# Performance work log

Measured on AMD Instinct MI355X. Metric: run time of the kernel, lower is better.

Reference implementation:

```python
import jax, jax.numpy as jnp
import numpy as np

N = 100000   # nodes (in_ch)
D = 128      # emb_ch
E = 1600000  # nonzeros in A_hat
RATE = 0.1   # dropout rate


def setup_inputs() -> dict:
    key = jax.random.key(0)
    k1, k2, k3, k4, k5, k6 = jax.random.split(key, 6)
    x = jnp.arange(N, dtype=jnp.int64) if jax.config.jax_enable_x64 else jnp.arange(N, dtype=jnp.int32)
    rows = jax.random.randint(k1, (E,), 0, N)
    cols = jax.random.randint(k2, (E,), 0, N)
    A_vals = jax.random.uniform(k3, (E,), dtype=jnp.float32)
    # xavier_uniform for [N, D]: bound = sqrt(6/(N+D))
    bound = float(np.sqrt(6.0 / (N + D)))
    emb_weight = jax.random.uniform(k4, (N, D), jnp.float32, -bound, bound)
    u1 = jax.random.uniform(k5, (N, D), dtype=jnp.float32)
    u2 = jax.random.uniform(k6, (N, D), dtype=jnp.float32)
    return {"x": x, "rows": rows, "cols": cols, "A_vals": A_vals,
            "emb_weight": emb_weight, "u1": u1, "u2": u2}


def _dropout(h, u):
    keep = (u >= RATE).astype(h.dtype)
    return h * keep / (1.0 - RATE)


def _spmm(rows, cols, vals, h):
    # out[i] = sum_{e: rows[e]==i} vals[e] * h[cols[e]]  -- COO SpMM
    msgs = vals[:, None] * h[cols]  # [E, D]
    return jax.ops.segment_sum(msgs, rows, num_segments=N)


def reference(x, rows, cols, A_vals, emb_weight, u1, u2):
    h0 = emb_weight[x]                       # embedding lookup [N, D]
    h1 = _spmm(rows, cols, A_vals, _dropout(h0, u1))
    h2 = _spmm(rows, cols, A_vals, _dropout(h1, u2))
    return (h0 + h1 + h2) / 3.0
```

## Files before the change

### kernel.cpp

```cpp
#include <hip/hip_runtime.h>

#define DD 128
#define SCAN_CHUNK 1024

struct __align__(8) Edge { int c; float v; };

__device__ __forceinline__ unsigned short f2bf(float f) {
    unsigned int u = __float_as_uint(f);
    u = u + 0x7fffu + ((u >> 16) & 1u);
    return (unsigned short)(u >> 16);
}
__device__ __forceinline__ float bf_lo(unsigned int p) { return __uint_as_float(p << 16); }
__device__ __forceinline__ float bf_hi(unsigned int p) { return __uint_as_float(p & 0xffff0000u); }


__global__ __launch_bounds__(256) void k_zero(int* __restrict__ p, int n) {
    int i = blockIdx.x * 256 + threadIdx.x;
    if (i < n) p[i] = 0;
}

__global__ __launch_bounds__(256) void k_hist(const int* __restrict__ rows,
                                              int* __restrict__ cnt,
                                              int* __restrict__ rank, int E) {
    int e = blockIdx.x * 256 + threadIdx.x;
    if (e < E) rank[e] = atomicAdd(&cnt[rows[e]], 1);
}

__global__ __launch_bounds__(256) void k_scan1(int* __restrict__ data,
                                               int* __restrict__ bsum, int n) {
    __shared__ int s[256];
    int tid = threadIdx.x;
    int base = blockIdx.x * SCAN_CHUNK + tid * 4;
    int v0 = 0, v1 = 0, v2 = 0, v3 = 0;
    if (base + 0 < n) v0 = data[base + 0];
    if (base + 1 < n) v1 = data[base + 1];
    if (base + 2 < n) v2 = data[base + 2];
    if (base + 3 < n) v3 = data[base + 3];
    int tsum = v0 + v1 + v2 + v3;
    s[tid] = tsum;
    __syncthreads();
    for (int off = 1; off < 256; off <<= 1) {
        int t = (tid >= off) ? s[tid - off] : 0;
        __syncthreads();
        s[tid] += t;
        __syncthreads();
    }
    int excl = s[tid] - tsum;
    if (tid == 255) bsum[blockIdx.x] = s[255];
    if (base + 0 < n) data[base + 0] = excl;
    if (base + 1 < n) data[base + 1] = excl + v0;
    if (base + 2 < n) data[base + 2] = excl + v0 + v1;
    if (base + 3 < n) data[base + 3] = excl + v0 + v1 + v2;
}

__global__ __launch_bounds__(256) void k_scan23(int* __restrict__ data,
                                                const int* __restrict__ bsum,
                                                int nb, int n) {
    __shared__ int s[1024];
    int tid = threadIdx.x;
    for (int i = tid; i < nb; i += 256) s[i] = bsum[i];
    __syncthreads();
    if (tid == 0) {
        int run = 0;
        for (int i = 0; i < nb; ++i) { int t = s[i]; s[i] = run; run += t; }
    }
    __syncthreads();
    int i = blockIdx.x * 256 + tid;
    if (i < n) data[i] += s[i >> 10];
}

__global__ __launch_bounds__(256) void k_scatter(const int* __restrict__ rows,
                                                 const int* __restrict__ cols,
                                                 const float* __restrict__ vals,
                                                 const int* __restrict__ rowstart,
                                                 const int* __restrict__ rank,
                                                 Edge* __restrict__ ev, int E) {
    int e = blockIdx.x * 256 + threadIdx.x;
    if (e >= E) return;
    int r = rows[e];
    Edge ed;
    ed.c = cols[e];
    ed.v = vals[e];
    ev[rowstart[r] + rank[e]] = ed;
}


__global__ __launch_bounds__(256) void k_drop_bf(const float* __restrict__ src,
                                                 const float* __restrict__ u,
                                                 ushort* __restrict__ g, int total4) {
    int i = blockIdx.x * 256 + threadIdx.x;
    if (i >= total4) return;
    float4 h = ((const float4*)src)[i];
    float4 uu = ((const float4*)u)[i];
    const float s = 1.0f / 0.9f;
    ushort4 o;
    o.x = f2bf((uu.x >= 0.1f) ? h.x * s : 0.0f);
    o.y = f2bf((uu.y >= 0.1f) ? h.y * s : 0.0f);
    o.z = f2bf((uu.z >= 0.1f) ? h.z * s : 0.0f);
    o.w = f2bf((uu.w >= 0.1f) ? h.w * s : 0.0f);
    ((ushort4*)g)[i] = o;
}

template <int MODE>
__global__ __launch_bounds__(256) void k_gather(const int* __restrict__ rowstart,
                                                const Edge* __restrict__ ev,
                                                const ushort* __restrict__ srcb,
                                                const float* __restrict__ u2,
                                                const float* __restrict__ emb,
                                                const float* __restrict__ h1in,
                                                float* __restrict__ dst,
                                                ushort* __restrict__ g2,
                                                int N, int E) {
    int t = blockIdx.x * 256 + threadIdx.x;
    int row = t >> 5;
    int lane = t & 31;
    if (row >= N) return;
    int start = rowstart[row];
    int end = (row == N - 1) ? E : rowstart[row + 1];
    const uint2* s2 = (const uint2*)srcb;
    float ax = 0.f, ay = 0.f, az = 0.f, aw = 0.f;
    int e = start;
    for (; e + 4 <= end; e += 4) {
        Edge e0 = ev[e + 0];
        Edge e1 = ev[e + 1];
        Edge e2 = ev[e + 2];
        Edge e3 = ev[e + 3];
        uint2 p0 = s2[((size_t)e0.c << 5) + lane];
        uint2 p1 = s2[((size_t)e1.c << 5) + lane];
        uint2 p2 = s2[((size_t)e2.c << 5) + lane];
        uint2 p3 = s2[((size_t)e3.c << 5) + lane];
        ax = fmaf(e0.v, bf_lo(p0.x), ax); ay = fmaf(e0.v, bf_hi(p0.x), ay);
        az = fmaf(e0.v, bf_lo(p0.y), az); aw = fmaf(e0.v, bf_hi(p0.y), aw);
        ax = fmaf(e1.v, bf_lo(p1.x), ax); ay = fmaf(e1.v, bf_hi(p1.x), ay);
        az = fmaf(e1.v, bf_lo(p1.y), az); aw = fmaf(e1.v, bf_hi(p1.y), aw);
        ax = fmaf(e2.v, bf_lo(p2.x), ax); ay = fmaf(e2.v, bf_hi(p2.x), ay);
        az = fmaf(e2.v, bf_lo(p2.y), az); aw = fmaf(e2.v, bf_hi(p2.y), aw);
        ax = fmaf(e3.v, bf_lo(p3.x), ax); ay = fmaf(e3.v, bf_hi(p3.x), ay);
        az = fmaf(e3.v, bf_lo(p3.y), az); aw = fmaf(e3.v, bf_hi(p3.y), aw);
    }
    for (; e < end; ++e) {
        Edge ed = ev[e];
        uint2 p = s2[((size_t)ed.c << 5) + lane];
        ax = fmaf(ed.v, bf_lo(p.x), ax); ay = fmaf(ed.v, bf_hi(p.x), ay);
        az = fmaf(ed.v, bf_lo(p.y), az); aw = fmaf(ed.v, bf_hi(p.y), aw);
    }
    size_t o = ((size_t)row << 7) + (size_t)lane * 4;
    if (MODE == 1) {
        *(float4*)(dst + o) = make_float4(ax, ay, az, aw);
        float4 uu = *(const float4*)(u2 + o);
        const float s = 1.0f / 0.9f;
        ushort4 gg;
        gg.x = f2bf((uu.x >= 0.1f) ? ax * s : 0.0f);
        gg.y = f2bf((uu.y >= 0.1f) ? ay * s : 0.0f);
        gg.z = f2bf((uu.z >= 0.1f) ? az * s : 0.0f);
        gg.w = f2bf((uu.w >= 0.1f) ? aw * s : 0.0f);
        *(ushort4*)(g2 + o) = gg;
    } else {
        float4 e4 = *(const float4*)(emb + o);
        float4 h4 = *(const float4*)(h1in + o);
        const float t3 = 1.0f / 3.0f;
        float4 r;
        r.x = (e4.x + h4.x + ax) * t3;
        r.y = (e4.y + h4.y + ay) * t3;
        r.z = (e4.z + h4.z + az) * t3;
        r.w = (e4.w + h4.w + aw) * t3;
        *(float4*)(dst + o) = r;
    }
}


extern "C" void kernel_launch(void* const* d_in, const int* in_sizes, int n_in,
                              void* d_out, int out_size, void* d_ws, size_t ws_size,
                              hipStream_t stream) {
    const int* rows = (const int*)d_in[1];
    const int* cols = (const int*)d_in[2];
    const float* vals = (const float*)d_in[3];
    const float* emb = (const float*)d_in[4];
    const float* u1 = (const float*)d_in[5];
    const float* u2 = (const float*)d_in[6];
    float* out = (float*)d_out;

    const int N = in_sizes[0];
    const int E = in_sizes[1];
    const size_t ND = (size_t)N * DD;

    char* ws = (char*)d_ws;
    ushort* g1 = (ushort*)ws;  ws += ND * sizeof(ushort);
    ushort* g2 = (ushort*)ws;  ws += ND * sizeof(ushort);
    float* h1  = (float*)ws;   ws += ND * sizeof(float);
    int* cnt   = (int*)ws;     ws += (size_t)N * sizeof(int);
    int* rank  = (int*)ws;     ws += (size_t)E * sizeof(int);
    Edge* ev   = (Edge*)ws;    ws += (size_t)E * sizeof(Edge);
    int* bsum  = (int*)ws;

    const int total4 = (int)(ND / 4);
    const int gridElem = (total4 + 255) / 256;
    const int gridE = (E + 255) / 256;
    const int gridN = (N + 255) / 256;
    const int nScanBlocks = (N + SCAN_CHUNK - 1) / SCAN_CHUNK;
    const int gridRow = (int)(((size_t)N * 32 + 255) / 256);

    k_zero<<<gridN, 256, 0, stream>>>(cnt, N);
    k_hist<<<gridE, 256, 0, stream>>>(rows, cnt, rank, E);
    k_scan1<<<nScanBlocks, 256, 0, stream>>>(cnt, bsum, N);
    k_scan23<<<gridN, 256, 0, stream>>>(cnt, bsum, nScanBlocks, N);
    k_scatter<<<gridE, 256, 0, stream>>>(rows, cols, vals, cnt, rank, ev, E);

    k_drop_bf<<<gridElem, 256, 0, stream>>>(emb, u1, g1, total4);
    k_gather<1><<<gridRow, 256, 0, stream>>>(cnt, ev, g1, u2, nullptr, nullptr, h1, g2, N, E);
    k_gather<2><<<gridRow, 256, 0, stream>>>(cnt, ev, g2, nullptr, emb, h1, out, nullptr, N, E);
}
```

Measured before the change: 452.7 us.

## Switch gathered features to fp16, widen gather lanes, add nontemporal loads/stores

Stores the dropout-applied features and the intermediate h1 as fp16 instead of bf16/fp32, which halves the h1 round trip. The gather kernel now uses 16 lanes per row, each loading 16 bytes (8 halves), and unrolls by 8 edges to put more loads in flight. Nontemporal load/store hints are added across the preprocessing, dropout and epilogue streams. Storing h1 in fp16 adds rounding error to the final output, and fp16 has a narrower exponent range than bf16.

```diff
diff --git a/kernel.cpp b/kernel.cpp
--- a/kernel.cpp
+++ b/kernel.cpp
@@ -1,17 +1,28 @@
 #include <hip/hip_runtime.h>
+#include <hip/hip_fp16.h>
 
 #define DD 128
 #define SCAN_CHUNK 1024
 
+typedef float          f32x4 __attribute__((ext_vector_type(4)));
+typedef unsigned int   u32x4 __attribute__((ext_vector_type(4)));
+typedef unsigned int   u32x2 __attribute__((ext_vector_type(2)));
+typedef unsigned short u16x8 __attribute__((ext_vector_type(8)));
+
 struct __align__(8) Edge { int c; float v; };
 
-__device__ __forceinline__ unsigned short f2bf(float f) {
-    unsigned int u = __float_as_uint(f);
-    u = u + 0x7fffu + ((u >> 16) & 1u);
-    return (unsigned short)(u >> 16);
-}
-__device__ __forceinline__ float bf_lo(unsigned int p) { return __uint_as_float(p << 16); }
-__device__ __forceinline__ float bf_hi(unsigned int p) { return __uint_as_float(p & 0xffff0000u); }
+__device__ __forceinline__ unsigned short f2h(float f) {
+    return __half_as_ushort(__float2half(f));
+}
+__device__ __forceinline__ float2 up2(unsigned int u) {
+    __half2 h = *reinterpret_cast<const __half2*>(&u);
+    return __half22float2(h);
+}
+
+template <typename T>
+__device__ __forceinline__ T ldnt(const T* p) { return __builtin_nontemporal_load(p); }
+template <typename T>
+__device__ __forceinline__ void stnt(T* p, T v) { __builtin_nontemporal_store(v, p); }
 
 
 __global__ __launch_bounds__(256) void k_zero(int* __restrict__ p, int n) {
@@ -23,7 +34,11 @@
                                               int* __restrict__ cnt,
                                               int* __restrict__ rank, int E) {
     int e = blockIdx.x * 256 + threadIdx.x;
-    if (e < E) rank[e] = atomicAdd(&cnt[rows[e]], 1);
+    if (e < E) {
+        int r = ldnt(rows + e);
+        int old = atomicAdd(&cnt[r], 1);
+        stnt(rank + e, old);
+    }
 }
 
 __global__ __launch_bounds__(256) void k_scan1(int* __restrict__ data,
@@ -77,94 +92,125 @@
                                                  Edge* __restrict__ ev, int E) {
     int e = blockIdx.x * 256 + threadIdx.x;
     if (e >= E) return;
-    int r = rows[e];
+    int r = ldnt(rows + e);
     Edge ed;
-    ed.c = cols[e];
-    ed.v = vals[e];
+    ed.c = ldnt(cols + e);
+    ed.v = ldnt(vals + e);
     ev[rowstart[r] + rank[e]] = ed;
 }
 
 
-__global__ __launch_bounds__(256) void k_drop_bf(const float* __restrict__ src,
-                                                 const float* __restrict__ u,
-                                                 ushort* __restrict__ g, int total4) {
+__global__ __launch_bounds__(256) void k_drop_h(const float* __restrict__ src,
+                                                const float* __restrict__ u,
+                                                ushort* __restrict__ g, int total8) {
     int i = blockIdx.x * 256 + threadIdx.x;
-    if (i >= total4) return;
-    float4 h = ((const float4*)src)[i];
-    float4 uu = ((const float4*)u)[i];
+    if (i >= total8) return;
+    const f32x4* s4 = (const f32x4*)src;
+    const f32x4* u4 = (const f32x4*)u;
+    f32x4 hA = ldnt(s4 + 2 * (size_t)i);
+    f32x4 hB = ldnt(s4 + 2 * (size_t)i + 1);
+    f32x4 uA = ldnt(u4 + 2 * (size_t)i);
+    f32x4 uB = ldnt(u4 + 2 * (size_t)i + 1);
     const float s = 1.0f / 0.9f;
-    ushort4 o;
-    o.x = f2bf((uu.x >= 0.1f) ? h.x * s : 0.0f);
-    o.y = f2bf((uu.y >= 0.1f) ? h.y * s : 0.0f);
-    o.z = f2bf((uu.z >= 0.1f) ? h.z * s : 0.0f);
-    o.w = f2bf((uu.w >= 0.1f) ? h.w * s : 0.0f);
-    ((ushort4*)g)[i] = o;
+    u16x8 o;
+    o[0] = f2h((uA.x >= 0.1f) ? hA.x * s : 0.0f);
+    o[1] = f2h((uA.y >= 0.1f) ? hA.y * s : 0.0f);
+    o[2] = f2h((uA.z >= 0.1f) ? hA.z * s : 0.0f);
+    o[3] = f2h((uA.w >= 0.1f) ? hA.w * s : 0.0f);
+    o[4] = f2h((uB.x >= 0.1f) ? hB.x * s : 0.0f);
+    o[5] = f2h((uB.y >= 0.1f) ? hB.y * s : 0.0f);
+    o[6] = f2h((uB.z >= 0.1f) ? hB.z * s : 0.0f);
+    o[7] = f2h((uB.w >= 0.1f) ? hB.w * s : 0.0f);
+    ((u16x8*)g)[i] = o;
 }
 
 template <int MODE>
 __global__ __launch_bounds__(256) void k_gather(const int* __restrict__ rowstart,
                                                 const Edge* __restrict__ ev,
-                                                const ushort* __restrict__ srcb,
+                                                const ushort* __restrict__ srch,
                                                 const float* __restrict__ u2,
                                                 const float* __restrict__ emb,
-                                                const float* __restrict__ h1in,
-                                                float* __restrict__ dst,
+                                                const ushort* __restrict__ p16in,
+                                                ushort* __restrict__ p16out,
                                                 ushort* __restrict__ g2,
+                                                float* __restrict__ out,
                                                 int N, int E) {
     int t = blockIdx.x * 256 + threadIdx.x;
-    int row = t >> 5;
-    int lane = t & 31;
+    int row = t >> 4;
+    int lane = t & 15;
     if (row >= N) return;
     int start = rowstart[row];
     int end = (row == N - 1) ? E : rowstart[row + 1];
-    const uint2* s2 = (const uint2*)srcb;
-    float ax = 0.f, ay = 0.f, az = 0.f, aw = 0.f;
+    const u32x4* __restrict__ s4 = (const u32x4*)srch;
+    float a0 = 0.f, a1 = 0.f, a2 = 0.f, a3 = 0.f;
+    float a4 = 0.f, a5 = 0.f, a6 = 0.f, a7 = 0.f;
+
+#define LDE(i) Edge E##i; { u32x2 q_ = ldnt((const u32x2*)(ev + e + i)); \
+                            E##i.c = (int)q_.x; E##i.v = __uint_as_float(q_.y); }
+#define GQ(i)  u32x4 q##i = s4[((size_t)E##i.c << 4) + lane];
+#define ACC(i) { float vv = E##i.v; \
+        float2 w0 = up2(q##i.x), w1 = up2(q##i.y), w2 = up2(q##i.z), w3 = up2(q##i.w); \
+        a0 = fmaf(vv, w0.x, a0); a1 = fmaf(vv, w0.y, a1); \
+        a2 = fmaf(vv, w1.x, a2); a3 = fmaf(vv, w1.y, a3); \
+        a4 = fmaf(vv, w2.x, a4); a5 = fmaf(vv, w2.y, a5); \
+        a6 = fmaf(vv, w3.x, a6); a7 = fmaf(vv, w3.y, a7); }
+
     int e = start;
-    for (; e + 4 <= end; e += 4) {
-        Edge e0 = ev[e + 0];
-        Edge e1 = ev[e + 1];
-        Edge e2 = ev[e + 2];
-        Edge e3 = ev[e + 3];
-        uint2 p0 = s2[((size_t)e0.c << 5) + lane];
-        uint2 p1 = s2[((size_t)e1.c << 5) + lane];
-        uint2 p2 = s2[((size_t)e2.c << 5) + lane];
-        uint2 p3 = s2[((size_t)e3.c << 5) + lane];
-        ax = fmaf(e0.v, bf_lo(p0.x), ax); ay = fmaf(e0.v, bf_hi(p0.x), ay);
-        az = fmaf(e0.v, bf_lo(p0.y), az); aw = fmaf(e0.v, bf_hi(p0.y), aw);
-        ax = fmaf(e1.v, bf_lo(p1.x), ax); ay = fmaf(e1.v, bf_hi(p1.x), ay);
-        az = fmaf(e1.v, bf_lo(p1.y), az); aw = fmaf(e1.v, bf_hi(p1.y), aw);
-        ax = fmaf(e2.v, bf_lo(p2.x), ax); ay = fmaf(e2.v, bf_hi(p2.x), ay);
-        az = fmaf(e2.v, bf_lo(p2.y), az); aw = fmaf(e2.v, bf_hi(p2.y), aw);
-        ax = fmaf(e3.v, bf_lo(p3.x), ax); ay = fmaf(e3.v, bf_hi(p3.x), ay);
-        az = fmaf(e3.v, bf_lo(p3.y), az); aw = fmaf(e3.v, bf_hi(p3.y), aw);
+    for (; e + 8 <= end; e += 8) {
+        LDE(0) LDE(1) LDE(2) LDE(3) LDE(4) LDE(5) LDE(6) LDE(7)
+        GQ(0) GQ(1) GQ(2) GQ(3) GQ(4) GQ(5) GQ(6) GQ(7)
+        ACC(0) ACC(1) ACC(2) ACC(3) ACC(4) ACC(5) ACC(6) ACC(7)
+    }
+    if (e + 4 <= end) {
+        LDE(0) LDE(1) LDE(2) LDE(3)
+        GQ(0) GQ(1) GQ(2) GQ(3)
+        ACC(0) ACC(1) ACC(2) ACC(3)
+        e += 4;
     }
     for (; e < end; ++e) {
-        Edge ed = ev[e];
-        uint2 p = s2[((size_t)ed.c << 5) + lane];
-        ax = fmaf(ed.v, bf_lo(p.x), ax); ay = fmaf(ed.v, bf_hi(p.x), ay);
-        az = fmaf(ed.v, bf_lo(p.y), az); aw = fmaf(ed.v, bf_hi(p.y), aw);
-    }
-    size_t o = ((size_t)row << 7) + (size_t)lane * 4;
+        LDE(0) GQ(0) ACC(0)
+    }
+#undef LDE
+#undef GQ
+#undef ACC
+
+    size_t o = ((size_t)row << 7) + (size_t)lane * 8;
     if (MODE == 1) {
-        *(float4*)(dst + o) = make_float4(ax, ay, az, aw);
-        float4 uu = *(const float4*)(u2 + o);
+        const f32x4* u4 = (const f32x4*)(u2 + o);
+        f32x4 uA = ldnt(u4);
+        f32x4 uB = ldnt(u4 + 1);
         const float s = 1.0f / 0.9f;
-        ushort4 gg;
-        gg.x = f2bf((uu.x >= 0.1f) ? ax * s : 0.0f);
-        gg.y = f2bf((uu.y >= 0.1f) ? ay * s : 0.0f);
-        gg.z = f2bf((uu.z >= 0.1f) ? az * s : 0.0f);
-        gg.w = f2bf((uu.w >= 0.1f) ? aw * s : 0.0f);
-        *(ushort4*)(g2 + o) = gg;
+        u16x8 gg;
+        gg[0] = f2h((uA.x >= 0.1f) ? a0 * s : 0.0f);
+        gg[1] = f2h((uA.y >= 0.1f) ? a1 * s : 0.0f);
+        gg[2] = f2h((uA.z >= 0.1f) ? a2 * s : 0.0f);
+        gg[3] = f2h((uA.w >= 0.1f) ? a3 * s : 0.0f);
+        gg[4] = f2h((uB.x >= 0.1f) ? a4 * s : 0.0f);
+        gg[5] = f2h((uB.y >= 0.1f) ? a5 * s : 0.0f);
+        gg[6] = f2h((uB.z >= 0.1f) ? a6 * s : 0.0f);
+        gg[7] = f2h((uB.w >= 0.1f) ? a7 * s : 0.0f);
+        stnt((u16x8*)(g2 + o), gg);
+        u16x8 pp;
+        pp[0] = f2h(a0); pp[1] = f2h(a1); pp[2] = f2h(a2); pp[3] = f2h(a3);
+        pp[4] = f2h(a4); pp[5] = f2h(a5); pp[6] = f2h(a6); pp[7] = f2h(a7);
+        stnt((u16x8*)(p16out + o), pp);
     } else {
-        float4 e4 = *(const float4*)(emb + o);
-        float4 h4 = *(const float4*)(h1in + o);
+        f32x4 eA = ldnt((const f32x4*)(emb + o));
+        f32x4 eB = ldnt((const f32x4*)(emb + o) + 1);
+        u32x4 pq = ldnt((const u32x4*)(p16in + o));
+        float2 p0 = up2(pq.x), p1 = up2(pq.y), p2 = up2(pq.z), p3 = up2(pq.w);
         const float t3 = 1.0f / 3.0f;
-        float4 r;
-        r.x = (e4.x + h4.x + ax) * t3;
-        r.y = (e4.y + h4.y + ay) * t3;
-        r.z = (e4.z + h4.z + az) * t3;
-        r.w = (e4.w + h4.w + aw) * t3;
-        *(float4*)(dst + o) = r;
+        f32x4 rA, rB;
+        rA.x = (eA.x + p0.x + a0) * t3;
+        rA.y = (eA.y + p0.y + a1) * t3;
+        rA.z = (eA.z + p1.x + a2) * t3;
+        rA.w = (eA.w + p1.y + a3) * t3;
+        rB.x = (eB.x + p2.x + a4) * t3;
+        rB.y = (eB.y + p2.y + a5) * t3;
+        rB.z = (eB.z + p3.x + a6) * t3;
+        rB.w = (eB.w + p3.y + a7) * t3;
+        stnt((f32x4*)(out + o), rA);
+        stnt((f32x4*)(out + o) + 1, rB);
     }
 }
 
@@ -185,20 +231,20 @@
     const size_t ND = (size_t)N * DD;
 
     char* ws = (char*)d_ws;
-    ushort* g1 = (ushort*)ws;  ws += ND * sizeof(ushort);
-    ushort* g2 = (ushort*)ws;  ws += ND * sizeof(ushort);
-    float* h1  = (float*)ws;   ws += ND * sizeof(float);
-    int* cnt   = (int*)ws;     ws += (size_t)N * sizeof(int);
-    int* rank  = (int*)ws;     ws += (size_t)E * sizeof(int);
-    Edge* ev   = (Edge*)ws;    ws += (size_t)E * sizeof(Edge);
-    int* bsum  = (int*)ws;
-
-    const int total4 = (int)(ND / 4);
-    const int gridElem = (total4 + 255) / 256;
+    ushort* g1  = (ushort*)ws; ws += ND * sizeof(ushort);
+    ushort* g2  = (ushort*)ws; ws += ND * sizeof(ushort);
+    ushort* p16 = (ushort*)ws; ws += ND * sizeof(ushort);
+    int* cnt    = (int*)ws;    ws += (size_t)N * sizeof(int);
+    int* rank   = (int*)ws;    ws += (size_t)E * sizeof(int);
+    Edge* ev    = (Edge*)ws;   ws += (size_t)E * sizeof(Edge);
+    int* bsum   = (int*)ws;
+
+    const int total8 = (int)(ND / 8);
+    const int gridDrop = (total8 + 255) / 256;
     const int gridE = (E + 255) / 256;
     const int gridN = (N + 255) / 256;
     const int nScanBlocks = (N + SCAN_CHUNK - 1) / SCAN_CHUNK;
-    const int gridRow = (int)(((size_t)N * 32 + 255) / 256);
+    const int gridRow = (int)(((size_t)N * 16 + 255) / 256);
 
     k_zero<<<gridN, 256, 0, stream>>>(cnt, N);
     k_hist<<<gridE, 256, 0, stream>>>(rows, cnt, rank, E);
@@ -206,7 +252,9 @@
     k_scan23<<<gridN, 256, 0, stream>>>(cnt, bsum, nScanBlocks, N);
     k_scatter<<<gridE, 256, 0, stream>>>(rows, cols, vals, cnt, rank, ev, E);
 
-    k_drop_bf<<<gridElem, 256, 0, stream>>>(emb, u1, g1, total4);
-    k_gather<1><<<gridRow, 256, 0, stream>>>(cnt, ev, g1, u2, nullptr, nullptr, h1, g2, N, E);
-    k_gather<2><<<gridRow, 256, 0, stream>>>(cnt, ev, g2, nullptr, emb, h1, out, nullptr, N, E);
-}
+    k_drop_h<<<gridDrop, 256, 0, stream>>>(emb, u1, g1, total8);
+    k_gather<1><<<gridRow, 256, 0, stream>>>(cnt, ev, g1, u2, nullptr, nullptr,
+                                             p16, g2, nullptr, N, E);
+    k_gather<2><<<gridRow, 256, 0, stream>>>(cnt, ev, g2, nullptr, emb, p16,
+                                             nullptr, nullptr, out, N, E);
+}
```

Result: faster. 439.4 us (-2.9%).
